# Optimization experiments

Hardware: AMD Instinct MI355X
Metric: run time of the kernel (lower is better)

## Reference

```python
import jax, jax.numpy as jnp
import numpy as np

B, N, M = 2, 131072, 512
VOXEL_SIZE = 0.5
SCALE = 10.0          # points lie in [0, SCALE)^3
G = 20                # static voxels per axis: ceil(SCALE / VOXEL_SIZE)
V = G * G * G         # total voxels per batch element


def setup_inputs() -> dict:
    key = jax.random.key(0)
    kx, ks = jax.random.split(key)
    x = jax.random.uniform(kx, (B, N, 3), dtype=jnp.float32) * SCALE
    # random_sample_point_cloud: sample M point indices without replacement per batch
    perm = jax.vmap(lambda k: jax.random.permutation(k, N))(jax.random.split(ks, B))
    sampled_idx = perm[:, :M].astype(jnp.int32)
    return {"x": x, "sampled_idx": sampled_idx}


def _voxel_idx(pts, min_coords):
    # metric_to_voxel_space: floor((p - min) / voxel_size), clipped to the grid
    idx = jnp.floor((pts - min_coords[:, None, :]) / VOXEL_SIZE).astype(jnp.int32)
    return jnp.clip(idx, 0, G - 1)  # (B, n, 3)


def reference(x, sampled_idx):
    # --- estimate_normal_distributions_with_size: per-voxel mean + covariance ---
    min_coords = x.min(axis=1)                                     # (B, 3)
    vox = _voxel_idx(x, min_coords)                                # (B, N, 3)
    flat = (vox[..., 0] * G + vox[..., 1]) * G + vox[..., 2]       # (B, N) flat voxel id

    seg = (flat + jnp.arange(B, dtype=flat.dtype)[:, None] * V).reshape(-1)  # global seg ids
    pts = x.reshape(-1, 3)
    cnt = jax.ops.segment_sum(jnp.ones((B * N,), jnp.float32), seg,
                              num_segments=B * V).reshape(B, V, 1)
    s1 = jax.ops.segment_sum(pts, seg, num_segments=B * V).reshape(B, V, 3)
    outer = (pts[:, :, None] * pts[:, None, :]).reshape(-1, 9)
    s2 = jax.ops.segment_sum(outer, seg, num_segments=B * V).reshape(B, V, 9)

    safe = jnp.maximum(cnt, 1.0)                                   # empty voxels -> zeros
    mean = s1 / safe                                               # (B, V, 3)
    cov = s2 / safe - (mean[:, :, :, None] * mean[:, :, None, :]).reshape(B, V, 9)
    dists = jnp.concatenate([mean, cov], axis=-1)                  # (B, V, 12)

    # --- gather distributions at the sampled points' voxels ---
    sflat = jnp.take_along_axis(flat, sampled_idx.astype(jnp.int32), axis=1)   # (B, M)
    filtered = jnp.take_along_axis(dists, sflat[..., None], axis=1)            # (B, M, 12)
    return filtered
```

## Files before the change

kernel.cpp:

```cpp
#include <hip/hip_runtime.h>

#define BB 2
#define NN 131072
#define MM 512
#define GG 20
#define VV (GG * GG * GG)
#define NBLKX 128

#define OFF_PARTIAL 0
#define OFF_MINV    3072
#define OFF_SFLAT   3200
#define OFF_FLAGS   8192
#define OFF_SUMS    24576
#define ZWORDS      ((16384 + 640000) / 4)

__device__ __forceinline__ int vox_coord(float p, float mn) {
    int i = (int)floorf((p - mn) * 2.0f);
    return min(max(i, 0), GG - 1);
}

__global__ __launch_bounds__(256) void vox_min(const float* __restrict__ x,
                                               char* __restrict__ ws) {
    const int b = blockIdx.y;
    const int tid = blockIdx.x * 256 + threadIdx.x;
    const int gtid = (b * NBLKX + blockIdx.x) * 256 + threadIdx.x;

    {
        int* z = (int*)(ws + OFF_FLAGS);
        for (int i = gtid; i < ZWORDS; i += NBLKX * BB * 256) z[i] = 0;
    }

    const float4* xb = (const float4*)(x + (size_t)b * NN * 3);
    float4 f0 = xb[3 * tid + 0];
    float4 f1 = xb[3 * tid + 1];
    float4 f2 = xb[3 * tid + 2];
    float mx = fminf(fminf(f0.x, f0.w), fminf(f1.z, f2.y));
    float my = fminf(fminf(f0.y, f1.x), fminf(f1.w, f2.z));
    float mz = fminf(fminf(f0.z, f1.y), fminf(f2.x, f2.w));

    for (int off = 32; off > 0; off >>= 1) {
        mx = fminf(mx, __shfl_down(mx, off, 64));
        my = fminf(my, __shfl_down(my, off, 64));
        mz = fminf(mz, __shfl_down(mz, off, 64));
    }
    __shared__ float lmin[4][3];
    int wave = threadIdx.x >> 6;
    if ((threadIdx.x & 63) == 0) {
        lmin[wave][0] = mx; lmin[wave][1] = my; lmin[wave][2] = mz;
    }
    __syncthreads();
    if (threadIdx.x == 0) {
        float* pm = (float*)(ws + OFF_PARTIAL) + (b * NBLKX + blockIdx.x) * 3;
        pm[0] = fminf(fminf(lmin[0][0], lmin[1][0]), fminf(lmin[2][0], lmin[3][0]));
        pm[1] = fminf(fminf(lmin[0][1], lmin[1][1]), fminf(lmin[2][1], lmin[3][1]));
        pm[2] = fminf(fminf(lmin[0][2], lmin[1][2]), fminf(lmin[2][2], lmin[3][2]));
    }
}

__global__ __launch_bounds__(1024) void vox_mark(const float* __restrict__ x,
                                                 const int* __restrict__ sidx,
                                                 char* __restrict__ ws) {
    __shared__ float smin[BB][3];
    const int t = threadIdx.x;

    if (t < 384) {
        int pair = t >> 6;
        int lane = t & 63;
        int pb = pair / 3, axis = pair % 3;
        const float* pm = (const float*)(ws + OFF_PARTIAL);
        float m = fminf(pm[(pb * NBLKX + lane) * 3 + axis],
                        pm[(pb * NBLKX + lane + 64) * 3 + axis]);
        for (int off = 32; off > 0; off >>= 1)
            m = fminf(m, __shfl_down(m, off, 64));
        if (lane == 0) {
            smin[pb][axis] = m;
            ((float*)(ws + OFF_MINV))[pb * 3 + axis] = m;
        }
    }
    __syncthreads();

    int b = t >> 9;
    int pi = sidx[t];
    const float* p = x + ((size_t)b * NN + pi) * 3;
    int ix = vox_coord(p[0], smin[b][0]);
    int iy = vox_coord(p[1], smin[b][1]);
    int iz = vox_coord(p[2], smin[b][2]);
    int flat = (ix * GG + iy) * GG + iz;
    ((int*)(ws + OFF_SFLAT))[t] = flat;
    ((unsigned char*)(ws + OFF_FLAGS))[b * VV + flat] = 1;
}

__global__ __launch_bounds__(256) void vox_accum(const float* __restrict__ x,
                                                 char* __restrict__ ws) {
    const int b = blockIdx.y;
    const int tid = blockIdx.x * 256 + threadIdx.x;
    const float* mv = (const float*)(ws + OFF_MINV) + b * 3;
    const float mnx = mv[0], mny = mv[1], mnz = mv[2];
    const unsigned char* flags = (const unsigned char*)(ws + OFF_FLAGS) + b * VV;
    float* sums = (float*)(ws + OFF_SUMS) + (size_t)b * VV * 10;

    const float4* xb = (const float4*)(x + (size_t)b * NN * 3);
    float4 f0 = xb[3 * tid + 0];
    float4 f1 = xb[3 * tid + 1];
    float4 f2 = xb[3 * tid + 2];
    float px[4] = {f0.x, f0.w, f1.z, f2.y};
    float py[4] = {f0.y, f1.x, f1.w, f2.z};
    float pz[4] = {f0.z, f1.y, f2.x, f2.w};
#pragma unroll
    for (int k = 0; k < 4; ++k) {
        int ix = vox_coord(px[k], mnx);
        int iy = vox_coord(py[k], mny);
        int iz = vox_coord(pz[k], mnz);
        int flat = (ix * GG + iy) * GG + iz;
        if (flags[flat]) {
            float* s = sums + (size_t)flat * 10;
            atomicAdd(s + 0, 1.0f);
            atomicAdd(s + 1, px[k]);
            atomicAdd(s + 2, py[k]);
            atomicAdd(s + 3, pz[k]);
            atomicAdd(s + 4, px[k] * px[k]);
            atomicAdd(s + 5, px[k] * py[k]);
            atomicAdd(s + 6, px[k] * pz[k]);
            atomicAdd(s + 7, py[k] * py[k]);
            atomicAdd(s + 8, py[k] * pz[k]);
            atomicAdd(s + 9, pz[k] * pz[k]);
        }
    }
}

__global__ __launch_bounds__(256) void vox_final(const char* __restrict__ ws,
                                                 float* __restrict__ out) {
    int t = blockIdx.x * 256 + threadIdx.x;
    if (t >= BB * MM) return;
    int b = t >> 9;
    int flat = ((const int*)(ws + OFF_SFLAT))[t];
    const float* s = (const float*)(ws + OFF_SUMS) + ((size_t)b * VV + flat) * 10;
    float cnt = s[0];
    float inv = 1.0f / fmaxf(cnt, 1.0f);
    float mx = s[1] * inv, my = s[2] * inv, mz = s[3] * inv;
    float cxx = s[4] * inv - mx * mx;
    float cxy = s[5] * inv - mx * my;
    float cxz = s[6] * inv - mx * mz;
    float cyy = s[7] * inv - my * my;
    float cyz = s[8] * inv - my * mz;
    float czz = s[9] * inv - mz * mz;
    float* o = out + (size_t)t * 12;
    o[0] = mx;  o[1] = my;  o[2] = mz;
    o[3] = cxx; o[4] = cxy; o[5] = cxz;
    o[6] = cxy; o[7] = cyy; o[8] = cyz;
    o[9] = cxz; o[10] = cyz; o[11] = czz;
}

extern "C" void kernel_launch(void* const* d_in, const int* in_sizes, int n_in,
                              void* d_out, int out_size, void* d_ws, size_t ws_size,
                              hipStream_t stream) {
    const float* x = (const float*)d_in[0];
    const int* sidx = (const int*)d_in[1];
    float* out = (float*)d_out;
    char* ws = (char*)d_ws;

    vox_min<<<dim3(NBLKX, BB), 256, 0, stream>>>(x, ws);
    vox_mark<<<1, 1024, 0, stream>>>(x, sidx, ws);
    vox_accum<<<dim3(NBLKX, BB), 256, 0, stream>>>(x, ws);
    vox_final<<<(BB * MM + 255) / 256, 256, 0, stream>>>(ws, out);
}
```

Before: 80.58 us.

## Fuse four voxel kernels into one cooperative kernel with grid syncs

```diff
diff --git a/kernel.cpp b/kernel.cpp
--- a/kernel.cpp
+++ b/kernel.cpp
@@ -1,154 +1,147 @@
 #include <hip/hip_runtime.h>
+#include <hip/hip_cooperative_groups.h>
+
+namespace cg = cooperative_groups;
 
 #define BB 2
 #define NN 131072
 #define MM 512
 #define GG 20
 #define VV (GG * GG * GG)
-#define NBLKX 128
+#define NBLK 128
+#define NTHR 512
 
 #define OFF_PARTIAL 0
-#define OFF_MINV    3072
-#define OFF_SFLAT   3200
+#define OFF_SFLAT   1536
 #define OFF_FLAGS   8192
 #define OFF_SUMS    24576
-#define ZWORDS      ((16384 + 640000) / 4)
+#define ZINT4       41024
 
 __device__ __forceinline__ int vox_coord(float p, float mn) {
     int i = (int)floorf((p - mn) * 2.0f);
     return min(max(i, 0), GG - 1);
 }
 
-__global__ __launch_bounds__(256) void vox_min(const float* __restrict__ x,
-                                               char* __restrict__ ws) {
-    const int b = blockIdx.y;
-    const int tid = blockIdx.x * 256 + threadIdx.x;
-    const int gtid = (b * NBLKX + blockIdx.x) * 256 + threadIdx.x;
+__global__ __launch_bounds__(NTHR, 1) void vox_fused(const float* __restrict__ x,
+                                                     const int* __restrict__ sidx,
+                                                     char* __restrict__ ws,
+                                                     float* __restrict__ out) {
+    cg::grid_group grid = cg::this_grid();
+    const int t = threadIdx.x;
+    const int gtid = blockIdx.x * NTHR + t;
+    const int b = gtid >> 15;
 
-    {
-        int* z = (int*)(ws + OFF_FLAGS);
-        for (int i = gtid; i < ZWORDS; i += NBLKX * BB * 256) z[i] = 0;
-    }
+    __shared__ float lmin[8][3];
+    __shared__ float smin[BB][3];
 
-    const float4* xb = (const float4*)(x + (size_t)b * NN * 3);
-    float4 f0 = xb[3 * tid + 0];
-    float4 f1 = xb[3 * tid + 1];
-    float4 f2 = xb[3 * tid + 2];
-    float mx = fminf(fminf(f0.x, f0.w), fminf(f1.z, f2.y));
-    float my = fminf(fminf(f0.y, f1.x), fminf(f1.w, f2.z));
-    float mz = fminf(fminf(f0.z, f1.y), fminf(f2.x, f2.w));
+    if (gtid < ZINT4)
+        ((int4*)(ws + OFF_FLAGS))[gtid] = make_int4(0, 0, 0, 0);
 
+    const float4* xb = (const float4*)x;
+    float4 f0 = xb[3 * gtid + 0];
+    float4 f1 = xb[3 * gtid + 1];
+    float4 f2 = xb[3 * gtid + 2];
+    float px[4] = {f0.x, f0.w, f1.z, f2.y};
+    float py[4] = {f0.y, f1.x, f1.w, f2.z};
+    float pz[4] = {f0.z, f1.y, f2.x, f2.w};
+
+    float mx = fminf(fminf(px[0], px[1]), fminf(px[2], px[3]));
+    float my = fminf(fminf(py[0], py[1]), fminf(py[2], py[3]));
+    float mz = fminf(fminf(pz[0], pz[1]), fminf(pz[2], pz[3]));
     for (int off = 32; off > 0; off >>= 1) {
         mx = fminf(mx, __shfl_down(mx, off, 64));
         my = fminf(my, __shfl_down(my, off, 64));
         mz = fminf(mz, __shfl_down(mz, off, 64));
     }
-    __shared__ float lmin[4][3];
-    int wave = threadIdx.x >> 6;
-    if ((threadIdx.x & 63) == 0) {
-        lmin[wave][0] = mx; lmin[wave][1] = my; lmin[wave][2] = mz;
+    const int wave = t >> 6;
+    if ((t & 63) == 0) { lmin[wave][0] = mx; lmin[wave][1] = my; lmin[wave][2] = mz; }
+    __syncthreads();
+    if (t == 0) {
+        float ax = lmin[0][0], ay = lmin[0][1], az = lmin[0][2];
+#pragma unroll
+        for (int w = 1; w < 8; ++w) {
+            ax = fminf(ax, lmin[w][0]);
+            ay = fminf(ay, lmin[w][1]);
+            az = fminf(az, lmin[w][2]);
+        }
+        float* pm = (float*)(ws + OFF_PARTIAL) + blockIdx.x * 3;
+        pm[0] = ax; pm[1] = ay; pm[2] = az;
+    }
+
+    grid.sync();
+
+    if (t < 384) {
+        const int pair = t >> 6, lane = t & 63;
+        const int pb = pair / 3, axis = pair % 3;
+        const float* pm = (const float*)(ws + OFF_PARTIAL);
+        float m = pm[(pb * 64 + lane) * 3 + axis];
+        for (int off = 32; off > 0; off >>= 1)
+            m = fminf(m, __shfl_down(m, off, 64));
+        if (lane == 0) smin[pb][axis] = m;
     }
     __syncthreads();
-    if (threadIdx.x == 0) {
-        float* pm = (float*)(ws + OFF_PARTIAL) + (b * NBLKX + blockIdx.x) * 3;
-        pm[0] = fminf(fminf(lmin[0][0], lmin[1][0]), fminf(lmin[2][0], lmin[3][0]));
-        pm[1] = fminf(fminf(lmin[0][1], lmin[1][1]), fminf(lmin[2][1], lmin[3][1]));
-        pm[2] = fminf(fminf(lmin[0][2], lmin[1][2]), fminf(lmin[2][2], lmin[3][2]));
+    if (t < 8) {
+        const int j = blockIdx.x * 8 + t;
+        const int mb = j >> 9;
+        const int pi = sidx[j];
+        const float* p = x + ((size_t)mb * NN + pi) * 3;
+        int ix = vox_coord(p[0], smin[mb][0]);
+        int iy = vox_coord(p[1], smin[mb][1]);
+        int iz = vox_coord(p[2], smin[mb][2]);
+        int flat = (ix * GG + iy) * GG + iz;
+        ((int*)(ws + OFF_SFLAT))[j] = flat;
+        ((unsigned char*)(ws + OFF_FLAGS))[mb * VV + flat] = 1;
     }
-}
 
-__global__ __launch_bounds__(1024) void vox_mark(const float* __restrict__ x,
-                                                 const int* __restrict__ sidx,
-                                                 char* __restrict__ ws) {
-    __shared__ float smin[BB][3];
-    const int t = threadIdx.x;
+    grid.sync();
 
-    if (t < 384) {
-        int pair = t >> 6;
-        int lane = t & 63;
-        int pb = pair / 3, axis = pair % 3;
-        const float* pm = (const float*)(ws + OFF_PARTIAL);
-        float m = fminf(pm[(pb * NBLKX + lane) * 3 + axis],
-                        pm[(pb * NBLKX + lane + 64) * 3 + axis]);
-        for (int off = 32; off > 0; off >>= 1)
-            m = fminf(m, __shfl_down(m, off, 64));
-        if (lane == 0) {
-            smin[pb][axis] = m;
-            ((float*)(ws + OFF_MINV))[pb * 3 + axis] = m;
+    {
+        const float mnx = smin[b][0], mny = smin[b][1], mnz = smin[b][2];
+        const unsigned char* flags = (const unsigned char*)(ws + OFF_FLAGS) + b * VV;
+        float* sums = (float*)(ws + OFF_SUMS) + (size_t)b * VV * 10;
+#pragma unroll
+        for (int k = 0; k < 4; ++k) {
+            int ix = vox_coord(px[k], mnx);
+            int iy = vox_coord(py[k], mny);
+            int iz = vox_coord(pz[k], mnz);
+            int flat = (ix * GG + iy) * GG + iz;
+            if (flags[flat]) {
+                float* s = sums + (size_t)flat * 10;
+                unsafeAtomicAdd(s + 0, 1.0f);
+                unsafeAtomicAdd(s + 1, px[k]);
+                unsafeAtomicAdd(s + 2, py[k]);
+                unsafeAtomicAdd(s + 3, pz[k]);
+                unsafeAtomicAdd(s + 4, px[k] * px[k]);
+                unsafeAtomicAdd(s + 5, px[k] * py[k]);
+                unsafeAtomicAdd(s + 6, px[k] * pz[k]);
+                unsafeAtomicAdd(s + 7, py[k] * py[k]);
+                unsafeAtomicAdd(s + 8, py[k] * pz[k]);
+                unsafeAtomicAdd(s + 9, pz[k] * pz[k]);
+            }
         }
     }
-    __syncthreads();
 
-    int b = t >> 9;
-    int pi = sidx[t];
-    const float* p = x + ((size_t)b * NN + pi) * 3;
-    int ix = vox_coord(p[0], smin[b][0]);
-    int iy = vox_coord(p[1], smin[b][1]);
-    int iz = vox_coord(p[2], smin[b][2]);
-    int flat = (ix * GG + iy) * GG + iz;
-    ((int*)(ws + OFF_SFLAT))[t] = flat;
-    ((unsigned char*)(ws + OFF_FLAGS))[b * VV + flat] = 1;
-}
+    grid.sync();
 
-__global__ __launch_bounds__(256) void vox_accum(const float* __restrict__ x,
-                                                 char* __restrict__ ws) {
-    const int b = blockIdx.y;
-    const int tid = blockIdx.x * 256 + threadIdx.x;
-    const float* mv = (const float*)(ws + OFF_MINV) + b * 3;
-    const float mnx = mv[0], mny = mv[1], mnz = mv[2];
-    const unsigned char* flags = (const unsigned char*)(ws + OFF_FLAGS) + b * VV;
-    float* sums = (float*)(ws + OFF_SUMS) + (size_t)b * VV * 10;
-
-    const float4* xb = (const float4*)(x + (size_t)b * NN * 3);
-    float4 f0 = xb[3 * tid + 0];
-    float4 f1 = xb[3 * tid + 1];
-    float4 f2 = xb[3 * tid + 2];
-    float px[4] = {f0.x, f0.w, f1.z, f2.y};
-    float py[4] = {f0.y, f1.x, f1.w, f2.z};
-    float pz[4] = {f0.z, f1.y, f2.x, f2.w};
-#pragma unroll
-    for (int k = 0; k < 4; ++k) {
-        int ix = vox_coord(px[k], mnx);
-        int iy = vox_coord(py[k], mny);
-        int iz = vox_coord(pz[k], mnz);
-        int flat = (ix * GG + iy) * GG + iz;
-        if (flags[flat]) {
-            float* s = sums + (size_t)flat * 10;
-            atomicAdd(s + 0, 1.0f);
-            atomicAdd(s + 1, px[k]);
-            atomicAdd(s + 2, py[k]);
-            atomicAdd(s + 3, pz[k]);
-            atomicAdd(s + 4, px[k] * px[k]);
-            atomicAdd(s + 5, px[k] * py[k]);
-            atomicAdd(s + 6, px[k] * pz[k]);
-            atomicAdd(s + 7, py[k] * py[k]);
-            atomicAdd(s + 8, py[k] * pz[k]);
-            atomicAdd(s + 9, pz[k] * pz[k]);
-        }
+    if (gtid < BB * MM) {
+        const int mb = gtid >> 9;
+        const int flat = ((const int*)(ws + OFF_SFLAT))[gtid];
+        const float* s = (const float*)(ws + OFF_SUMS) + ((size_t)mb * VV + flat) * 10;
+        float cnt = s[0];
+        float inv = 1.0f / fmaxf(cnt, 1.0f);
+        float mxm = s[1] * inv, mym = s[2] * inv, mzm = s[3] * inv;
+        float cxx = s[4] * inv - mxm * mxm;
+        float cxy = s[5] * inv - mxm * mym;
+        float cxz = s[6] * inv - mxm * mzm;
+        float cyy = s[7] * inv - mym * mym;
+        float cyz = s[8] * inv - mym * mzm;
+        float czz = s[9] * inv - mzm * mzm;
+        float* o = out + (size_t)gtid * 12;
+        o[0] = mxm; o[1] = mym; o[2] = mzm;
+        o[3] = cxx; o[4] = cxy; o[5] = cxz;
+        o[6] = cxy; o[7] = cyy; o[8] = cyz;
+        o[9] = cxz; o[10] = cyz; o[11] = czz;
     }
-}
-
-__global__ __launch_bounds__(256) void vox_final(const char* __restrict__ ws,
-                                                 float* __restrict__ out) {
-    int t = blockIdx.x * 256 + threadIdx.x;
-    if (t >= BB * MM) return;
-    int b = t >> 9;
-    int flat = ((const int*)(ws + OFF_SFLAT))[t];
-    const float* s = (const float*)(ws + OFF_SUMS) + ((size_t)b * VV + flat) * 10;
-    float cnt = s[0];
-    float inv = 1.0f / fmaxf(cnt, 1.0f);
-    float mx = s[1] * inv, my = s[2] * inv, mz = s[3] * inv;
-    float cxx = s[4] * inv - mx * mx;
-    float cxy = s[5] * inv - mx * my;
-    float cxz = s[6] * inv - mx * mz;
-    float cyy = s[7] * inv - my * my;
-    float cyz = s[8] * inv - my * mz;
-    float czz = s[9] * inv - mz * mz;
-    float* o = out + (size_t)t * 12;
-    o[0] = mx;  o[1] = my;  o[2] = mz;
-    o[3] = cxx; o[4] = cxy; o[5] = cxz;
-    o[6] = cxy; o[7] = cyy; o[8] = cyz;
-    o[9] = cxz; o[10] = cyz; o[11] = czz;
 }
 
 extern "C" void kernel_launch(void* const* d_in, const int* in_sizes, int n_in,
@@ -159,8 +152,7 @@
     float* out = (float*)d_out;
     char* ws = (char*)d_ws;
 
-    vox_min<<<dim3(NBLKX, BB), 256, 0, stream>>>(x, ws);
-    vox_mark<<<1, 1024, 0, stream>>>(x, sidx, ws);
-    vox_accum<<<dim3(NBLKX, BB), 256, 0, stream>>>(x, ws);
-    vox_final<<<(BB * MM + 255) / 256, 256, 0, stream>>>(ws, out);
+    void* args[] = {(void*)&x, (void*)&sidx, (void*)&ws, (void*)&out};
+    hipLaunchCooperativeKernel(reinterpret_cast<void*>(vox_fused),
+                               dim3(NBLK), dim3(NTHR), args, 0, stream);
 }
```

After: 133.0 us. 65.0% more time.
